# Kernel tuning notes

Hardware: AMD Instinct MI355X
Metric: run time of the kernel (lower is better)

The kernel has to match this reference:

```python
import jax, jax.numpy as jnp
import numpy as np

DIM = 1024
HEADS = 16
HEAD_DIM = DIM // HEADS
HIDDEN = 4 * DIM
EPS = 1e-5


def layer_norm(x, g, b):
    mu = jnp.mean(x, axis=-1, keepdims=True)
    var = jnp.var(x, axis=-1, keepdims=True)
    return (x - mu) * jax.lax.rsqrt(var + EPS) * g + b


def setup_inputs() -> dict:
    key = jax.random.key(0)
    ks = jax.random.split(key, 12)
    s = lambda k, shape, scale=0.02: (jax.random.normal(k, shape, jnp.float32) * scale)
    return {
        "tgt": jax.random.normal(ks[0], (4, 1024, DIM), jnp.float32),
        "emb_motion": jax.random.normal(ks[1], (4, 2048, DIM), jnp.float32),
        "ln_g": jnp.ones((DIM,), jnp.float32),
        "ln_b": jnp.zeros((DIM,), jnp.float32),
        "wq": s(ks[2], (DIM, DIM)), "bq": jnp.zeros((DIM,), jnp.float32),
        "wk": s(ks[3], (DIM, DIM)), "bk": jnp.zeros((DIM,), jnp.float32),
        "wv": s(ks[4], (DIM, DIM)), "bv": jnp.zeros((DIM,), jnp.float32),
        "wo": s(ks[5], (DIM, DIM)), "bo": jnp.zeros((DIM,), jnp.float32),
        "w1": s(ks[6], (DIM, HIDDEN)), "b1": jnp.zeros((HIDDEN,), jnp.float32),
        "w2": s(ks[7], (HIDDEN, DIM)), "b2": jnp.zeros((DIM,), jnp.float32),
    }


def reference(tgt, emb_motion, ln_g, ln_b, wq, bq, wk, bk, wv, bv, wo, bo, w1, b1, w2, b2):
    B, Nq, C = tgt.shape
    Nk = emb_motion.shape[1]
    temp = jnp.asarray(HEAD_DIM ** 0.5, tgt.dtype)

    # cross-attention: q = norm2(tgt); k = v = emb_motion (raw)
    qn = layer_norm(tgt, ln_g, ln_b)
    q = (qn @ wq + bq).reshape(B, Nq, HEADS, HEAD_DIM)
    k = (emb_motion @ wk + bk).reshape(B, Nk, HEADS, HEAD_DIM)
    v = (emb_motion @ wv + bv).reshape(B, Nk, HEADS, HEAD_DIM)

    scores = jnp.einsum("bqhd,bkhd->bhqk", q / temp, k)  # [B,H,Nq,Nk]
    attn = jax.nn.softmax(scores, axis=-1)
    ctx = jnp.einsum("bhqk,bkhd->bqhd", attn, v).reshape(B, Nq, C)
    tgt = tgt + (ctx @ wo + bo)

    # MLP block reuses the SAME norm2 params (as in the source)
    h = layer_norm(tgt, ln_g, ln_b)
    h = jax.nn.gelu(h @ w1 + b1, approximate=False)
    tgt = tgt + (h @ w2 + b2)
    return tgt
```

## Files before the change

### kernel.cpp

```cpp
#include <hip/hip_runtime.h>
#include <cstdint>
#include <cstddef>


typedef __attribute__((ext_vector_type(8))) short bf16x8;
typedef __attribute__((ext_vector_type(4))) float f32x4;

__device__ __forceinline__ short f2b(float f) {
    unsigned u = __builtin_bit_cast(unsigned, f);
    unsigned r = (u + 0x7FFFu + ((u >> 16) & 1u)) >> 16;
    return (short)r;
}

__device__ __forceinline__ f32x4 mfma16(bf16x8 a, bf16x8 b, f32x4 c) {
    return __builtin_amdgcn_mfma_f32_16x16x32_bf16(a, b, c, 0, 0, 0);
}

__device__ __forceinline__ void gload16(const void* g, void* l) {
    __builtin_amdgcn_global_load_lds(
        (const __attribute__((address_space(1))) unsigned int*)g,
        (__attribute__((address_space(3))) unsigned int*)l, 16, 0, 0);
}


__global__ __launch_bounds__(256) void transpose_f2b(
    const float* __restrict__ in, short* __restrict__ out, int R, int C) {
    __shared__ float tile[32][33];
    const int c0 = blockIdx.x * 32, r0 = blockIdx.y * 32;
    const int tx = threadIdx.x, ty = threadIdx.y;
#pragma unroll
    for (int i = 0; i < 4; ++i)
        tile[ty + 8 * i][tx] = in[(size_t)(r0 + ty + 8 * i) * C + c0 + tx];
    __syncthreads();
#pragma unroll
    for (int i = 0; i < 4; ++i)
        out[(size_t)(c0 + ty + 8 * i) * R + r0 + tx] = f2b(tile[tx][ty + 8 * i]);
}

__global__ __launch_bounds__(256) void conv_f2b(
    const float* __restrict__ in, short* __restrict__ out, int n4) {
    int i = blockIdx.x * 256 + threadIdx.x;
    if (i < n4) {
        float4 v = reinterpret_cast<const float4*>(in)[i];
        short4 o;
        o.x = f2b(v.x); o.y = f2b(v.y); o.z = f2b(v.z); o.w = f2b(v.w);
        reinterpret_cast<short4*>(out)[i] = o;
    }
}

__global__ __launch_bounds__(256) void ln_bf16(
    const float* __restrict__ x, const float* __restrict__ g,
    const float* __restrict__ bb, short* __restrict__ out) {
    const int row = blockIdx.x, tid = threadIdx.x;
    float4 v = reinterpret_cast<const float4*>(x + (size_t)row * 1024)[tid];
    float s = v.x + v.y + v.z + v.w;
    float q = v.x * v.x + v.y * v.y + v.z * v.z + v.w * v.w;
#pragma unroll
    for (int off = 32; off; off >>= 1) {
        s += __shfl_down(s, off);
        q += __shfl_down(q, off);
    }
    __shared__ float ss[4], sq[4];
    const int wave = tid >> 6, lane = tid & 63;
    if (lane == 0) { ss[wave] = s; sq[wave] = q; }
    __syncthreads();
    s = ss[0] + ss[1] + ss[2] + ss[3];
    q = sq[0] + sq[1] + sq[2] + sq[3];
    const float mu = s * (1.f / 1024.f);
    const float var = q * (1.f / 1024.f) - mu * mu;
    const float rs = rsqrtf(var + 1e-5f);
    float4 gg = reinterpret_cast<const float4*>(g)[tid];
    float4 bv = reinterpret_cast<const float4*>(bb)[tid];
    short4 o;
    o.x = f2b((v.x - mu) * rs * gg.x + bv.x);
    o.y = f2b((v.y - mu) * rs * gg.y + bv.y);
    o.z = f2b((v.z - mu) * rs * gg.z + bv.z);
    o.w = f2b((v.w - mu) * rs * gg.w + bv.w);
    reinterpret_cast<short4*>(out + (size_t)row * 1024)[tid] = o;
}

__global__ __launch_bounds__(256) void transpose_v(
    const short* __restrict__ vbuf, short* __restrict__ VT) {
    __shared__ short t[32][33];
    const int b = blockIdx.z >> 4, h = blockIdx.z & 15;
    const int n0 = blockIdx.x * 32, d0 = blockIdx.y * 32;
    const int tx = threadIdx.x, ty = threadIdx.y;
#pragma unroll
    for (int i = 0; i < 4; ++i)
        t[ty + 8 * i][tx] =
            vbuf[(size_t)(b * 2048 + n0 + ty + 8 * i) * 1024 + h * 64 + d0 + tx];
    __syncthreads();
#pragma unroll
    for (int i = 0; i < 4; ++i)
        VT[(size_t)((b * 16 + h) * 64 + d0 + ty + 8 * i) * 2048 + n0 + tx] =
            t[tx][ty + 8 * i];
}

template <int BIAS, int RESID, int GELU, int OUTF>
__global__ __launch_bounds__(256) void gemm_bt(
    const short* __restrict__ A, const short* __restrict__ BT,
    const float* __restrict__ bias, const float* __restrict__ resid,
    void* __restrict__ out, int M, int N, int K, float scale) {
    __shared__ __align__(16) short As[128 * 32];
    __shared__ __align__(16) short Bs[128 * 32];
    const int tid = threadIdx.x;
    const int wave = tid >> 6, lane = tid & 63;
    const int l15 = lane & 15, lhi = lane >> 4;
    const int bm = blockIdx.x, bn = blockIdx.y;
    const int wm = (wave >> 1) * 64, wn = (wave & 1) * 64;

    f32x4 acc[4][4];
#pragma unroll
    for (int i = 0; i < 4; ++i)
#pragma unroll
        for (int j = 0; j < 4; ++j) acc[i][j] = (f32x4){0.f, 0.f, 0.f, 0.f};

    for (int k0 = 0; k0 < K; k0 += 32) {
#pragma unroll
        for (int c = 0; c < 2; ++c) {
            const int ob = wave * 2048 + c * 1024;
            const int o = ob + lane * 16;
            const int row = o >> 6, kb = o & 63;
            const char* ga = (const char*)A + ((size_t)(bm * 128 + row) * K + k0) * 2 + kb;
            const char* gb = (const char*)BT + ((size_t)(bn * 128 + row) * K + k0) * 2 + kb;
            gload16(ga, (char*)As + ob);
            gload16(gb, (char*)Bs + ob);
        }
        __syncthreads();
        bf16x8 af[4], bfr[4];
#pragma unroll
        for (int t = 0; t < 4; ++t) {
            af[t]  = *(const bf16x8*)&As[(wm + t * 16 + l15) * 32 + lhi * 8];
            bfr[t] = *(const bf16x8*)&Bs[(wn + t * 16 + l15) * 32 + lhi * 8];
        }
#pragma unroll
        for (int mt = 0; mt < 4; ++mt)
#pragma unroll
            for (int nt = 0; nt < 4; ++nt)
                acc[mt][nt] = mfma16(af[mt], bfr[nt], acc[mt][nt]);
        __syncthreads();
    }

#pragma unroll
    for (int mt = 0; mt < 4; ++mt)
#pragma unroll
        for (int nt = 0; nt < 4; ++nt)
#pragma unroll
            for (int r = 0; r < 4; ++r) {
                const int row = bm * 128 + wm + mt * 16 + lhi * 4 + r;
                const int col = bn * 128 + wn + nt * 16 + l15;
                float v = acc[mt][nt][r];
                if (BIAS) v += bias[col];
                v *= scale;
                if (GELU) v = 0.5f * v * (1.f + erff(v * 0.70710678118f));
                if (RESID) v += resid[(size_t)row * N + col];
                if (OUTF)
                    ((float*)out)[(size_t)row * N + col] = v;
                else
                    ((short*)out)[(size_t)row * N + col] = f2b(v);
            }
}

__global__ __launch_bounds__(256) void attn_flash(
    const short* __restrict__ Q, const short* __restrict__ Kb,
    const short* __restrict__ VT, short* __restrict__ ctx) {
    __shared__ __align__(16) short kls[2 * 4096];
    __shared__ __align__(16) short vls[2 * 4096];
    __shared__ __align__(16) short pls[4 * 2304];
    const int tid = threadIdx.x, wave = tid >> 6, lane = tid & 63;
    const int l15 = lane & 15, lhi = lane >> 4;
    const int b = blockIdx.y >> 4, h = blockIdx.y & 15;
    const int q0 = blockIdx.x * 128 + wave * 32;

    bf16x8 qf[2][2];
#pragma unroll
    for (int f = 0; f < 2; ++f) {
        const short* qp = Q + ((size_t)(b * 1024 + q0 + f * 16 + l15) * 1024 + h * 64);
        qf[f][0] = *(const bf16x8*)(qp + lhi * 8);
        qf[f][1] = *(const bf16x8*)(qp + 32 + lhi * 8);
    }

    f32x4 oa[2][4];
#pragma unroll
    for (int f = 0; f < 2; ++f)
#pragma unroll
        for (int c = 0; c < 4; ++c) oa[f][c] = (f32x4){0.f, 0.f, 0.f, 0.f};
    float m[8], lsum[8];
#pragma unroll
    for (int i = 0; i < 8; ++i) { m[i] = -1e30f; lsum[i] = 0.f; }

    const int srow = (lane >> 3);
    const int scol = (((lane & 7) ^ srow) << 4);
    const int r0k = wave * 16 + srow;
    const int r1k = wave * 16 + 8 + srow;
    const char* kc0 = (const char*)(Kb + ((size_t)(b * 2048 + r0k) * 1024 + h * 64)) + scol;
    const char* kc1 = (const char*)(Kb + ((size_t)(b * 2048 + r1k) * 1024 + h * 64)) + scol;
    const char* vc0 = (const char*)(VT + ((size_t)((b * 16 + h) * 64 + r0k) * 2048)) + scol;
    const char* vc1 = (const char*)(VT + ((size_t)((b * 16 + h) * 64 + r1k) * 2048)) + scol;
    const int kdst0 = wave * 1024, kdst1 = wave * 1024 + 512;

    gload16(kc0, (char*)&kls[kdst0]);
    gload16(kc1, (char*)&kls[kdst1]);
    gload16(vc0, (char*)&vls[kdst0]);
    gload16(vc1, (char*)&vls[kdst1]);
    kc0 += 131072; kc1 += 131072; vc0 += 128; vc1 += 128;
    __syncthreads();

    short* plw = pls + wave * 2304;
    int cur = 0;

    for (int t = 0; t < 32; ++t) {
        const int nxt = cur ^ 1;
        if (t < 31) {
            gload16(kc0, (char*)&kls[nxt * 4096 + kdst0]);
            gload16(kc1, (char*)&kls[nxt * 4096 + kdst1]);
            gload16(vc0, (char*)&vls[nxt * 4096 + kdst0]);
            gload16(vc1, (char*)&vls[nxt * 4096 + kdst1]);
            kc0 += 131072; kc1 += 131072; vc0 += 128; vc1 += 128;
        }
        const char* kcur = (const char*)&kls[cur * 4096];
        const char* vcur = (const char*)&vls[cur * 4096];

        f32x4 s[2][4];
#pragma unroll
        for (int g = 0; g < 4; ++g) {
            const int key = g * 16 + l15;
            const int sw = (key & 7) << 4;
            const bf16x8 kf0 = *(const bf16x8*)(kcur + key * 128 + ((lhi * 16) ^ sw));
            const bf16x8 kf1 = *(const bf16x8*)(kcur + key * 128 + ((64 + lhi * 16) ^ sw));
            s[0][g] = mfma16(qf[0][0], kf0, (f32x4){0.f, 0.f, 0.f, 0.f});
            s[0][g] = mfma16(qf[0][1], kf1, s[0][g]);
            s[1][g] = mfma16(qf[1][0], kf0, (f32x4){0.f, 0.f, 0.f, 0.f});
            s[1][g] = mfma16(qf[1][1], kf1, s[1][g]);
        }

#pragma unroll
        for (int f = 0; f < 2; ++f)
#pragma unroll
            for (int r = 0; r < 4; ++r) {
                const int mi = f * 4 + r;
                float vm = fmaxf(fmaxf(s[f][0][r], s[f][1][r]),
                                 fmaxf(s[f][2][r], s[f][3][r]));
#pragma unroll
                for (int off = 1; off < 16; off <<= 1)
                    vm = fmaxf(vm, __shfl_xor(vm, off, 16));
                const float nm = fmaxf(m[mi], vm);
                const float sc = __expf(m[mi] - nm);
                m[mi] = nm;
                float ps = 0.f;
                const int prow = (f * 16 + lhi * 4 + r) * 72;
#pragma unroll
                for (int g = 0; g < 4; ++g) {
                    const float p = __expf(s[f][g][r] - nm);
                    ps += p;
                    plw[prow + g * 16 + l15] = f2b(p);
                }
                lsum[mi] = lsum[mi] * sc + ps;
                oa[f][0][r] *= sc; oa[f][1][r] *= sc;
                oa[f][2][r] *= sc; oa[f][3][r] *= sc;
            }

        bf16x8 vb[4][2];
#pragma unroll
        for (int ct = 0; ct < 4; ++ct) {
            const int d = ct * 16 + l15;
            const int sw = (d & 7) << 4;
            vb[ct][0] = *(const bf16x8*)(vcur + d * 128 + ((lhi * 16) ^ sw));
            vb[ct][1] = *(const bf16x8*)(vcur + d * 128 + ((64 + lhi * 16) ^ sw));
        }
#pragma unroll
        for (int f = 0; f < 2; ++f) {
            const bf16x8 pa0 = *(const bf16x8*)&plw[(f * 16 + l15) * 72 + lhi * 8];
            const bf16x8 pa1 = *(const bf16x8*)&plw[(f * 16 + l15) * 72 + 32 + lhi * 8];
#pragma unroll
            for (int ct = 0; ct < 4; ++ct) {
                oa[f][ct] = mfma16(pa0, vb[ct][0], oa[f][ct]);
                oa[f][ct] = mfma16(pa1, vb[ct][1], oa[f][ct]);
            }
        }
        __syncthreads();
        cur = nxt;
    }

#pragma unroll
    for (int i = 0; i < 8; ++i) {
#pragma unroll
        for (int off = 1; off < 16; off <<= 1)
            lsum[i] += __shfl_xor(lsum[i], off, 16);
        lsum[i] = 1.f / lsum[i];
    }
#pragma unroll
    for (int f = 0; f < 2; ++f)
#pragma unroll
        for (int r = 0; r < 4; ++r) {
            const int qrow = q0 + f * 16 + lhi * 4 + r;
            short* cp = ctx + ((size_t)(b * 1024 + qrow) * 1024 + h * 64);
            const float inv = lsum[f * 4 + r];
#pragma unroll
            for (int ct = 0; ct < 4; ++ct)
                cp[ct * 16 + l15] = f2b(oa[f][ct][r] * inv);
        }
}


extern "C" void kernel_launch(void* const* d_in, const int* in_sizes, int n_in,
                              void* d_out, int out_size, void* d_ws, size_t ws_size,
                              hipStream_t stream) {
    const float* tgt  = (const float*)d_in[0];
    const float* emb  = (const float*)d_in[1];
    const float* ln_g = (const float*)d_in[2];
    const float* ln_b = (const float*)d_in[3];
    const float* wq = (const float*)d_in[4];  const float* bq = (const float*)d_in[5];
    const float* wk = (const float*)d_in[6];  const float* bk = (const float*)d_in[7];
    const float* wv = (const float*)d_in[8];  const float* bv = (const float*)d_in[9];
    const float* wo = (const float*)d_in[10]; const float* bo = (const float*)d_in[11];
    const float* w1 = (const float*)d_in[12]; const float* b1 = (const float*)d_in[13];
    const float* w2 = (const float*)d_in[14]; const float* b2 = (const float*)d_in[15];

    char* ws = (char*)d_ws;
    const size_t MB = 1024 * 1024;
    short* wqT  = (short*)(ws + 0 * MB);
    short* wkT  = (short*)(ws + 2 * MB);
    short* wvT  = (short*)(ws + 4 * MB);
    short* woT  = (short*)(ws + 6 * MB);
    short* w1T  = (short*)(ws + 8 * MB);
    short* w2T  = (short*)(ws + 16 * MB);
    float* tgt2 = (float*)(ws + 24 * MB);
    short* embB = (short*)(ws + 40 * MB);
    short* qn   = (short*)(ws + 56 * MB);
    short* qbuf = (short*)(ws + 64 * MB);
    short* kbuf = (short*)(ws + 72 * MB);
    short* vbuf = (short*)(ws + 88 * MB);
    short* VT   = (short*)(ws + 104 * MB);
    short* ctx  = (short*)(ws + 120 * MB);
    short* h1   = (short*)(ws + 64 * MB);
    float* outp = (float*)d_out;

    const dim3 tb(32, 8);
    transpose_f2b<<<dim3(32, 32), tb, 0, stream>>>(wq, wqT, 1024, 1024);
    transpose_f2b<<<dim3(32, 32), tb, 0, stream>>>(wk, wkT, 1024, 1024);
    transpose_f2b<<<dim3(32, 32), tb, 0, stream>>>(wv, wvT, 1024, 1024);
    transpose_f2b<<<dim3(32, 32), tb, 0, stream>>>(wo, woT, 1024, 1024);
    transpose_f2b<<<dim3(128, 32), tb, 0, stream>>>(w1, w1T, 1024, 4096);
    transpose_f2b<<<dim3(32, 128), tb, 0, stream>>>(w2, w2T, 4096, 1024);
    conv_f2b<<<8192, 256, 0, stream>>>(emb, embB, 8192 * 1024 / 4);
    ln_bf16<<<4096, 256, 0, stream>>>(tgt, ln_g, ln_b, qn);
    gemm_bt<1, 0, 0, 0><<<dim3(32, 8), 256, 0, stream>>>(qn, wqT, bq, nullptr, qbuf, 4096, 1024, 1024, 0.125f);
    gemm_bt<1, 0, 0, 0><<<dim3(64, 8), 256, 0, stream>>>(embB, wkT, bk, nullptr, kbuf, 8192, 1024, 1024, 1.f);
    gemm_bt<1, 0, 0, 0><<<dim3(64, 8), 256, 0, stream>>>(embB, wvT, bv, nullptr, vbuf, 8192, 1024, 1024, 1.f);
    transpose_v<<<dim3(64, 2, 64), tb, 0, stream>>>(vbuf, VT);
    attn_flash<<<dim3(8, 64), 256, 0, stream>>>(qbuf, kbuf, VT, ctx);
    gemm_bt<1, 1, 0, 1><<<dim3(32, 8), 256, 0, stream>>>(ctx, woT, bo, tgt, tgt2, 4096, 1024, 1024, 1.f);
    ln_bf16<<<4096, 256, 0, stream>>>(tgt2, ln_g, ln_b, qn);
    gemm_bt<1, 0, 1, 0><<<dim3(32, 32), 256, 0, stream>>>(qn, w1T, b1, nullptr, h1, 4096, 4096, 1024, 1.f);
    gemm_bt<1, 1, 0, 1><<<dim3(32, 8), 256, 0, stream>>>(h1, w2T, b2, tgt2, outp, 4096, 1024, 4096, 1.f);

    (void)in_sizes; (void)n_in; (void)out_size; (void)ws_size;
}
```

Before: 563.4 us.

## Double K-step per GEMM barrier and halve attention rows per wave

The GEMM now loads two 32-wide K slices per iteration into separate LDS buffers, so there is one pair of barriers per 64 K instead of per 32. The attention kernel shrinks each wave to 16 query rows and doubles the grid to 1024 blocks, which gives more parallelism but means K/V tiles are reloaded twice as often. It also packs P to bf16 with v_cvt_pk_bf16_f32 into a swizzled, smaller P scratch buffer, and raises wave priority around the MFMA sections with s_setprio. The risks are extra global traffic for K/V in attention and less MFMA work per wave to hide latency.

```diff
diff --git a/kernel.cpp b/kernel.cpp
--- a/kernel.cpp
+++ b/kernel.cpp
@@ -101,8 +101,8 @@
     const short* __restrict__ A, const short* __restrict__ BT,
     const float* __restrict__ bias, const float* __restrict__ resid,
     void* __restrict__ out, int M, int N, int K, float scale) {
-    __shared__ __align__(16) short As[128 * 32];
-    __shared__ __align__(16) short Bs[128 * 32];
+    __shared__ __align__(16) short As[2][128 * 32];
+    __shared__ __align__(16) short Bs[2][128 * 32];
     const int tid = threadIdx.x;
     const int wave = tid >> 6, lane = tid & 63;
     const int l15 = lane & 15, lhi = lane >> 4;
@@ -115,29 +115,41 @@
 #pragma unroll
         for (int j = 0; j < 4; ++j) acc[i][j] = (f32x4){0.f, 0.f, 0.f, 0.f};
 
-    for (int k0 = 0; k0 < K; k0 += 32) {
-#pragma unroll
-        for (int c = 0; c < 2; ++c) {
-            const int ob = wave * 2048 + c * 1024;
-            const int o = ob + lane * 16;
-            const int row = o >> 6, kb = o & 63;
-            const char* ga = (const char*)A + ((size_t)(bm * 128 + row) * K + k0) * 2 + kb;
-            const char* gb = (const char*)BT + ((size_t)(bn * 128 + row) * K + k0) * 2 + kb;
-            gload16(ga, (char*)As + ob);
-            gload16(gb, (char*)Bs + ob);
+    const int ob0 = wave * 2048;
+    const int o0 = ob0 + lane * 16;
+    const int row0 = o0 >> 6, kb0 = o0 & 63;
+    const int ob1 = wave * 2048 + 1024;
+    const int o1 = ob1 + lane * 16;
+    const int row1 = o1 >> 6, kb1 = o1 & 63;
+
+    for (int k0 = 0; k0 < K; k0 += 64) {
+#pragma unroll
+        for (int hh = 0; hh < 2; ++hh) {
+            const int kc = k0 + hh * 32;
+            gload16((const char*)A + ((size_t)(bm * 128 + row0) * K + kc) * 2 + kb0,
+                    (char*)As[hh] + ob0);
+            gload16((const char*)A + ((size_t)(bm * 128 + row1) * K + kc) * 2 + kb1,
+                    (char*)As[hh] + ob1);
+            gload16((const char*)BT + ((size_t)(bn * 128 + row0) * K + kc) * 2 + kb0,
+                    (char*)Bs[hh] + ob0);
+            gload16((const char*)BT + ((size_t)(bn * 128 + row1) * K + kc) * 2 + kb1,
+                    (char*)Bs[hh] + ob1);
         }
         __syncthreads();
-        bf16x8 af[4], bfr[4];
-#pragma unroll
-        for (int t = 0; t < 4; ++t) {
-            af[t]  = *(const bf16x8*)&As[(wm + t * 16 + l15) * 32 + lhi * 8];
-            bfr[t] = *(const bf16x8*)&Bs[(wn + t * 16 + l15) * 32 + lhi * 8];
-        }
-#pragma unroll
-        for (int mt = 0; mt < 4; ++mt)
-#pragma unroll
-            for (int nt = 0; nt < 4; ++nt)
-                acc[mt][nt] = mfma16(af[mt], bfr[nt], acc[mt][nt]);
+#pragma unroll
+        for (int hh = 0; hh < 2; ++hh) {
+            bf16x8 af[4], bfr[4];
+#pragma unroll
+            for (int t = 0; t < 4; ++t) {
+                af[t]  = *(const bf16x8*)&As[hh][(wm + t * 16 + l15) * 32 + lhi * 8];
+                bfr[t] = *(const bf16x8*)&Bs[hh][(wn + t * 16 + l15) * 32 + lhi * 8];
+            }
+#pragma unroll
+            for (int mt = 0; mt < 4; ++mt)
+#pragma unroll
+                for (int nt = 0; nt < 4; ++nt)
+                    acc[mt][nt] = mfma16(af[mt], bfr[nt], acc[mt][nt]);
+        }
         __syncthreads();
     }
 
@@ -166,28 +178,21 @@
     const short* __restrict__ VT, short* __restrict__ ctx) {
     __shared__ __align__(16) short kls[2 * 4096];
     __shared__ __align__(16) short vls[2 * 4096];
-    __shared__ __align__(16) short pls[4 * 2304];
+    __shared__ __align__(16) short pls[4 * 1024];
     const int tid = threadIdx.x, wave = tid >> 6, lane = tid & 63;
     const int l15 = lane & 15, lhi = lane >> 4;
     const int b = blockIdx.y >> 4, h = blockIdx.y & 15;
-    const int q0 = blockIdx.x * 128 + wave * 32;
-
-    bf16x8 qf[2][2];
-#pragma unroll
-    for (int f = 0; f < 2; ++f) {
-        const short* qp = Q + ((size_t)(b * 1024 + q0 + f * 16 + l15) * 1024 + h * 64);
-        qf[f][0] = *(const bf16x8*)(qp + lhi * 8);
-        qf[f][1] = *(const bf16x8*)(qp + 32 + lhi * 8);
-    }
-
-    f32x4 oa[2][4];
-#pragma unroll
-    for (int f = 0; f < 2; ++f)
-#pragma unroll
-        for (int c = 0; c < 4; ++c) oa[f][c] = (f32x4){0.f, 0.f, 0.f, 0.f};
-    float m[8], lsum[8];
-#pragma unroll
-    for (int i = 0; i < 8; ++i) { m[i] = -1e30f; lsum[i] = 0.f; }
+    const int q0 = blockIdx.x * 64 + wave * 16;
+
+    const short* qp = Q + ((size_t)(b * 1024 + q0 + l15) * 1024 + h * 64);
+    const bf16x8 qf0 = *(const bf16x8*)(qp + lhi * 8);
+    const bf16x8 qf1 = *(const bf16x8*)(qp + 32 + lhi * 8);
+
+    f32x4 oa[4];
+#pragma unroll
+    for (int c = 0; c < 4; ++c) oa[c] = (f32x4){0.f, 0.f, 0.f, 0.f};
+    float m[4] = {-1e30f, -1e30f, -1e30f, -1e30f};
+    float lsum[4] = {0.f, 0.f, 0.f, 0.f};
 
     const int srow = (lane >> 3);
     const int scol = (((lane & 7) ^ srow) << 4);
@@ -206,7 +211,7 @@
     kc0 += 131072; kc1 += 131072; vc0 += 128; vc1 += 128;
     __syncthreads();
 
-    short* plw = pls + wave * 2304;
+    short* plw = pls + wave * 1024;
     int cur = 0;
 
     for (int t = 0; t < 32; ++t) {
@@ -221,44 +226,45 @@
         const char* kcur = (const char*)&kls[cur * 4096];
         const char* vcur = (const char*)&vls[cur * 4096];
 
-        f32x4 s[2][4];
+        f32x4 s[4];
+        __builtin_amdgcn_s_setprio(1);
 #pragma unroll
         for (int g = 0; g < 4; ++g) {
             const int key = g * 16 + l15;
             const int sw = (key & 7) << 4;
             const bf16x8 kf0 = *(const bf16x8*)(kcur + key * 128 + ((lhi * 16) ^ sw));
             const bf16x8 kf1 = *(const bf16x8*)(kcur + key * 128 + ((64 + lhi * 16) ^ sw));
-            s[0][g] = mfma16(qf[0][0], kf0, (f32x4){0.f, 0.f, 0.f, 0.f});
-            s[0][g] = mfma16(qf[0][1], kf1, s[0][g]);
-            s[1][g] = mfma16(qf[1][0], kf0, (f32x4){0.f, 0.f, 0.f, 0.f});
-            s[1][g] = mfma16(qf[1][1], kf1, s[1][g]);
-        }
-
-#pragma unroll
-        for (int f = 0; f < 2; ++f)
-#pragma unroll
-            for (int r = 0; r < 4; ++r) {
-                const int mi = f * 4 + r;
-                float vm = fmaxf(fmaxf(s[f][0][r], s[f][1][r]),
-                                 fmaxf(s[f][2][r], s[f][3][r]));
-#pragma unroll
-                for (int off = 1; off < 16; off <<= 1)
-                    vm = fmaxf(vm, __shfl_xor(vm, off, 16));
-                const float nm = fmaxf(m[mi], vm);
-                const float sc = __expf(m[mi] - nm);
-                m[mi] = nm;
-                float ps = 0.f;
-                const int prow = (f * 16 + lhi * 4 + r) * 72;
-#pragma unroll
-                for (int g = 0; g < 4; ++g) {
-                    const float p = __expf(s[f][g][r] - nm);
-                    ps += p;
-                    plw[prow + g * 16 + l15] = f2b(p);
-                }
-                lsum[mi] = lsum[mi] * sc + ps;
-                oa[f][0][r] *= sc; oa[f][1][r] *= sc;
-                oa[f][2][r] *= sc; oa[f][3][r] *= sc;
-            }
+            s[g] = mfma16(qf0, kf0, (f32x4){0.f, 0.f, 0.f, 0.f});
+            s[g] = mfma16(qf1, kf1, s[g]);
+        }
+        __builtin_amdgcn_s_setprio(0);
+
+#pragma unroll
+        for (int r = 0; r < 4; ++r) {
+            float vm = fmaxf(fmaxf(s[0][r], s[1][r]), fmaxf(s[2][r], s[3][r]));
+#pragma unroll
+            for (int off = 1; off < 16; off <<= 1)
+                vm = fmaxf(vm, __shfl_xor(vm, off, 16));
+            const float nm = fmaxf(m[r], vm);
+            const float sc = __expf(m[r] - nm);
+            m[r] = nm;
+            const float p0 = __expf(s[0][r] - nm);
+            const float p1 = __expf(s[1][r] - nm);
+            const float p2 = __expf(s[2][r] - nm);
+            const float p3 = __expf(s[3][r] - nm);
+            lsum[r] = lsum[r] * sc + ((p0 + p1) + (p2 + p3));
+            unsigned pk01, pk23;
+            asm("v_cvt_pk_bf16_f32 %0, %1, %2" : "=v"(pk01) : "v"(p0), "v"(p1));
+            asm("v_cvt_pk_bf16_f32 %0, %1, %2" : "=v"(pk23) : "v"(p2), "v"(p3));
+            const int prow = lhi * 4 + r;
+            char* prb = (char*)plw + prow * 128;
+            const int swp = (prow & 7) << 4;
+            *(short*)(prb + ((l15 * 2) ^ swp))      = (short)pk01;
+            *(short*)(prb + ((32 + l15 * 2) ^ swp)) = (short)(pk01 >> 16);
+            *(short*)(prb + ((64 + l15 * 2) ^ swp)) = (short)pk23;
+            *(short*)(prb + ((96 + l15 * 2) ^ swp)) = (short)(pk23 >> 16);
+            oa[0][r] *= sc; oa[1][r] *= sc; oa[2][r] *= sc; oa[3][r] *= sc;
+        }
 
         bf16x8 vb[4][2];
 #pragma unroll
@@ -268,38 +274,37 @@
             vb[ct][0] = *(const bf16x8*)(vcur + d * 128 + ((lhi * 16) ^ sw));
             vb[ct][1] = *(const bf16x8*)(vcur + d * 128 + ((64 + lhi * 16) ^ sw));
         }
-#pragma unroll
-        for (int f = 0; f < 2; ++f) {
-            const bf16x8 pa0 = *(const bf16x8*)&plw[(f * 16 + l15) * 72 + lhi * 8];
-            const bf16x8 pa1 = *(const bf16x8*)&plw[(f * 16 + l15) * 72 + 32 + lhi * 8];
-#pragma unroll
-            for (int ct = 0; ct < 4; ++ct) {
-                oa[f][ct] = mfma16(pa0, vb[ct][0], oa[f][ct]);
-                oa[f][ct] = mfma16(pa1, vb[ct][1], oa[f][ct]);
-            }
-        }
+        const char* prr = (const char*)plw + l15 * 128;
+        const int swr = (l15 & 7) << 4;
+        const bf16x8 pa0 = *(const bf16x8*)(prr + ((lhi * 16) ^ swr));
+        const bf16x8 pa1 = *(const bf16x8*)(prr + ((64 + lhi * 16) ^ swr));
+        __builtin_amdgcn_s_setprio(1);
+#pragma unroll
+        for (int ct = 0; ct < 4; ++ct) {
+            oa[ct] = mfma16(pa0, vb[ct][0], oa[ct]);
+            oa[ct] = mfma16(pa1, vb[ct][1], oa[ct]);
+        }
+        __builtin_amdgcn_s_setprio(0);
         __syncthreads();
         cur = nxt;
     }
 
 #pragma unroll
-    for (int i = 0; i < 8; ++i) {
+    for (int i = 0; i < 4; ++i) {
 #pragma unroll
         for (int off = 1; off < 16; off <<= 1)
             lsum[i] += __shfl_xor(lsum[i], off, 16);
         lsum[i] = 1.f / lsum[i];
     }
 #pragma unroll
-    for (int f = 0; f < 2; ++f)
-#pragma unroll
-        for (int r = 0; r < 4; ++r) {
-            const int qrow = q0 + f * 16 + lhi * 4 + r;
-            short* cp = ctx + ((size_t)(b * 1024 + qrow) * 1024 + h * 64);
-            const float inv = lsum[f * 4 + r];
-#pragma unroll
-            for (int ct = 0; ct < 4; ++ct)
-                cp[ct * 16 + l15] = f2b(oa[f][ct][r] * inv);
-        }
+    for (int r = 0; r < 4; ++r) {
+        const int qrow = q0 + lhi * 4 + r;
+        short* cp = ctx + ((size_t)(b * 1024 + qrow) * 1024 + h * 64);
+        const float inv = lsum[r];
+#pragma unroll
+        for (int ct = 0; ct < 4; ++ct)
+            cp[ct * 16 + l15] = f2b(oa[ct][r] * inv);
+    }
 }
 
 
@@ -349,7 +354,7 @@
     gemm_bt<1, 0, 0, 0><<<dim3(64, 8), 256, 0, stream>>>(embB, wkT, bk, nullptr, kbuf, 8192, 1024, 1024, 1.f);
     gemm_bt<1, 0, 0, 0><<<dim3(64, 8), 256, 0, stream>>>(embB, wvT, bv, nullptr, vbuf, 8192, 1024, 1024, 1.f);
     transpose_v<<<dim3(64, 2, 64), tb, 0, stream>>>(vbuf, VT);
-    attn_flash<<<dim3(8, 64), 256, 0, stream>>>(qbuf, kbuf, VT, ctx);
+    attn_flash<<<dim3(16, 64), 256, 0, stream>>>(qbuf, kbuf, VT, ctx);
     gemm_bt<1, 1, 0, 1><<<dim3(32, 8), 256, 0, stream>>>(ctx, woT, bo, tgt, tgt2, 4096, 1024, 1024, 1.f);
     ln_bf16<<<4096, 256, 0, stream>>>(tgt2, ln_g, ln_b, qn);
     gemm_bt<1, 0, 1, 0><<<dim3(32, 32), 256, 0, stream>>>(qn, w1T, b1, nullptr, h1, 4096, 4096, 1024, 1.f);
```

New measurement: 526.7 us. -6.5%, faster.
